# Optimization experiments

Hardware: AMD Instinct MI355X
Metric: run time of the kernel (lower is better)

Reference implementation:

```python
import jax, jax.numpy as jnp
import numpy as np

T, OBS, H, NOBJ = 32768, 256, 512, 4


def _xavier(key, shape):
    fan_in, fan_out = shape[0], shape[1]
    lim = jnp.sqrt(6.0 / (fan_in + fan_out)).astype(jnp.float32)
    return jax.random.uniform(key, shape, jnp.float32, -lim, lim)


def setup_inputs() -> dict:
    key = jax.random.key(0)
    ks = jax.random.split(key, 16)
    # weights stored as [in, out] so y = x @ W (same math as nn.Linear with W.T)
    return {
        "x": jax.random.normal(ks[0], (T, OBS), jnp.float32),
        "W_in0": _xavier(ks[1], (OBS, H)),
        "W_B0": _xavier(ks[2], (OBS, H)),
        "W_C0": _xavier(ks[3], (OBS, H)),
        "W_d0": _xavier(ks[4], (OBS, H)),
        "A_log0": jax.random.normal(ks[5], (H,), jnp.float32),
        "W_in1": _xavier(ks[6], (H, H)),
        "W_B1": _xavier(ks[7], (H, H)),
        "W_C1": _xavier(ks[8], (H, H)),
        "W_d1": _xavier(ks[9], (H, H)),
        "A_log1": jax.random.normal(ks[10], (H,), jnp.float32),
        "W_out": _xavier(ks[11], (H, NOBJ)),
        "b_out": jnp.zeros((NOBJ,), jnp.float32),
        "W_skip": _xavier(ks[12], (OBS, NOBJ)),
    }


def _mamba_layer(x, W_in, W_B, W_C, W_d, A_log):
    # x: [T, D_in] -> [T, H]
    x_state = x @ W_in           # [T, H]
    B = x @ W_B                  # [T, H]
    C = x @ W_C                  # [T, H]
    delta = jax.nn.sigmoid(x @ W_d)  # [T, H]
    A = -jnp.exp(A_log)          # [H]
    A_bar = jnp.exp(delta * A)   # [T, H], in (0, 1)
    Bx = B * x_state             # [T, H]

    def step(h, inp):
        a_t, bx_t = inp
        h = a_t * h + bx_t
        return h, h

    h0 = jnp.zeros((x_state.shape[-1],), x_state.dtype)
    _, h_seq = jax.lax.scan(step, h0, (A_bar, Bx))  # [T, H]
    return C * h_seq


def reference(x, W_in0, W_B0, W_C0, W_d0, A_log0,
              W_in1, W_B1, W_C1, W_d1, A_log1,
              W_out, b_out, W_skip):
    skip = x
    y = _mamba_layer(x, W_in0, W_B0, W_C0, W_d0, A_log0)
    y = _mamba_layer(y, W_in1, W_B1, W_C1, W_d1, A_log1)
    out = y @ W_out + b_out + skip @ W_skip  # [T, NOBJ]
    return out
```

## Files before the change

### kernel.cpp

```cpp
#include <hip/hip_runtime.h>

typedef __attribute__((ext_vector_type(8))) short short8;
typedef __attribute__((ext_vector_type(4))) float floatx4;

#define T_SIZE 32768
#define OBS    256
#define H      512
#define NC     1024
#define CHUNK  32
#define NGRP   64
#define GCH    16

__device__ __forceinline__ unsigned short f2bf(float f){
    union { float f; unsigned u; } v; v.f = f;
    unsigned u = v.u;
    u += 0x7FFFu + ((u >> 16) & 1u);
    return (unsigned short)(u >> 16);
}
__device__ __forceinline__ float bf2f(unsigned short u){
    union { unsigned u; float f; } v; v.u = ((unsigned)u) << 16; return v.f;
}

#define GLOAD_LDS16(g, l) \
    __builtin_amdgcn_global_load_lds((const __attribute__((address_space(1))) unsigned*)(g), \
                                     (__attribute__((address_space(3))) unsigned*)(l), 16, 0, 0)

__global__ void prep_kernel(const float* __restrict__ x, unsigned short* __restrict__ xb,
                            const float* __restrict__ A0W0, const float* __restrict__ A0W1,
                            const float* __restrict__ A0W2, const float* __restrict__ A0W3,
                            unsigned short* __restrict__ Wt0,
                            const float* __restrict__ A1W0, const float* __restrict__ A1W1,
                            const float* __restrict__ A1W2, const float* __restrict__ A1W3,
                            unsigned short* __restrict__ Wt1){
    const int b = blockIdx.x;
    const int tid = threadIdx.x;
    if (b < 8192){
        int i = b * 256 + tid;
        float4 v = ((const float4*)x)[i];
        ushort4 o;
        o.x = f2bf(v.x); o.y = f2bf(v.y); o.z = f2bf(v.z); o.w = f2bf(v.w);
        ((ushort4*)xb)[i] = o;
    } else if (b < 10240){
        const int K = OBS, KH = OBS * H;
        int idx = (b - 8192) * 256 + tid;
        int s   = idx / KH;
        int rem = idx - s * KH;
        int h = rem >> 8;
        int k = rem & 255;
        const float* W = (s == 0) ? A0W0 : (s == 1) ? A0W1 : (s == 2) ? A0W2 : A0W3;
        int bb = h >> 4, hh = h & 15;
        Wt0[(size_t)((bb * 4 + s) * 16 + hh) * K + k] = f2bf(W[(size_t)k * H + h]);
    } else {
        const int K = H, KH = H * H;
        int idx = (b - 10240) * 256 + tid;
        int s   = idx / KH;
        int rem = idx - s * KH;
        int h = rem >> 9;
        int k = rem & 511;
        const float* W = (s == 0) ? A1W0 : (s == 1) ? A1W1 : (s == 2) ? A1W2 : A1W3;
        int bb = h >> 4, hh = h & 15;
        Wt1[(size_t)((bb * 4 + s) * 16 + hh) * K + k] = f2bf(W[(size_t)k * H + h]);
    }
}

template<int K>
__global__ __launch_bounds__(256, 3) void gemm_layer_kernel(
    const unsigned short* __restrict__ xb,
    const unsigned short* __restrict__ wt,
    const float* __restrict__ A_log,
    unsigned short* __restrict__ gT, unsigned short* __restrict__ bxT, unsigned short* __restrict__ CT,
    float* __restrict__ Pbuf, float* __restrict__ Hbuf)
{
    __shared__ unsigned short SM[3][8192];

    const int tid  = threadIdx.x;
    const int wave = tid >> 6;
    const int lane = tid & 63;
    const int ml   = lane & 15;
    const int quad = lane >> 4;
    const int wm   = wave & 1;
    const int wn   = wave >> 1;

    const int flat = blockIdx.y * 16 + blockIdx.x;
    const int xcd  = flat & 7;
    const int j    = flat >> 3;
    const int nb   = j & 15;
    const int mb   = (j >> 4) * 8 + xcd;
    const int m0   = mb * 128;

    const int srow = tid >> 2;
    const int sel  = (((tid & 3) ^ ((tid >> 3) & 3))) * 8;
    const int swz  = (ml >> 1) & 3;

    const unsigned short* pa0 = xb + (size_t)(m0 + srow) * K + sel;
    const unsigned short* pa1 = pa0 + (size_t)64 * K;
    const unsigned short* pb0 = wt + (size_t)(nb * 128 + srow) * K + sel;
    const unsigned short* pb1 = pb0 + (size_t)64 * K;

    const int ldsA0 = (wave * 64 + 0  ) * 8;
    const int ldsA1 = (wave * 64 + 256) * 8;

    const int rbaseA = (wm * 64 + ml) * 32 + (quad ^ swz) * 8;
    const int rbaseB = (wn * 64 + ml) * 32 + (quad ^ swz) * 8;

    floatx4 acc[4][4];
    #pragma unroll
    for (int i = 0; i < 4; i++)
        #pragma unroll
        for (int jj = 0; jj < 4; jj++)
            acc[i][jj] = (floatx4)(0.0f);

    constexpr int NK = K >> 5;

#define STAGE(kt_) { const int b_ = (kt_) % 3; const int ko_ = (kt_) * 32; \
        GLOAD_LDS16(pa0 + ko_, &SM[b_][ldsA0]); \
        GLOAD_LDS16(pa1 + ko_, &SM[b_][ldsA1]); \
        GLOAD_LDS16(pb0 + ko_, &SM[b_][4096 + ldsA0]); \
        GLOAD_LDS16(pb1 + ko_, &SM[b_][4096 + ldsA1]); }

    STAGE(0); STAGE(1);
    asm volatile("s_waitcnt vmcnt(4)" ::: "memory");
    __builtin_amdgcn_s_barrier();
    __builtin_amdgcn_sched_barrier(0);

    #pragma unroll
    for (int kk = 0; kk < NK; ++kk){
        const int cur = kk % 3;

        if (kk + 2 < NK) STAGE(kk + 2);

        short8 av[4], bv[4];
        #pragma unroll
        for (int i = 0; i < 4; i++)
            av[i] = *(const short8*)(&SM[cur][0] + rbaseA + i * 16 * 32);
        #pragma unroll
        for (int jj = 0; jj < 4; jj++)
            bv[jj] = *(const short8*)(&SM[cur][4096] + rbaseB + jj * 16 * 32);

        __builtin_amdgcn_s_setprio(1);
        #pragma unroll
        for (int i = 0; i < 4; i++)
            #pragma unroll
            for (int jj = 0; jj < 4; jj++)
                acc[i][jj] = __builtin_amdgcn_mfma_f32_16x16x32_bf16(av[i], bv[jj], acc[i][jj], 0, 0, 0);
        __builtin_amdgcn_s_setprio(0);

        if (kk + 1 < NK){
            if (kk + 2 < NK) { asm volatile("s_waitcnt vmcnt(4)" ::: "memory"); }
            else             { asm volatile("s_waitcnt vmcnt(0)" ::: "memory"); }
            __builtin_amdgcn_s_barrier();
            __builtin_amdgcn_sched_barrier(0);
        }
    }
    __syncthreads();

#undef STAGE

    unsigned short* SMe = &SM[0][0];
    float2* segbuf = (float2*)(SMe + 12288);
    const int col = wn * 16 + ml;
    const int h   = nb * 32 + col;
    const float Aneg = -expf(A_log[h]);

    #pragma unroll
    for (int i = 0; i < 4; i++){
        float p = 1.0f, hh = 0.0f;
        #pragma unroll
        for (int r = 0; r < 4; r++){
            int trow = wm * 64 + i * 16 + quad * 4 + r;
            float dv = acc[i][3][r];
            float delta = 1.0f / (1.0f + expf(-dv));
            unsigned short gb = f2bf(delta * Aneg);
            float a = __expf(bf2f(gb));
            unsigned short bb = f2bf(acc[i][1][r] * acc[i][0][r]);
            SMe[        trow * 32 + col] = gb;
            SMe[4096 +  trow * 32 + col] = bb;
            SMe[8192 +  trow * 32 + col] = f2bf(acc[i][2][r]);
            hh = fmaf(a, hh, bf2f(bb));
            p *= a;
        }
        const int ch = wm * 2 + (i >> 1);
        const int s  = (i & 1) * 4 + quad;
        segbuf[(ch * 8 + s) * 32 + col] = make_float2(p, hh);
    }
    __syncthreads();
    {
        const short8* s8 = (const short8*)SMe;
        #pragma unroll
        for (int arr = 0; arr < 3; arr++){
            unsigned short* bp = (arr == 0) ? gT : (arr == 1) ? bxT : CT;
            #pragma unroll
            for (int half = 0; half < 2; half++){
                int u = half * 256 + tid;
                int row = u >> 2, part = u & 3;
                *(short8*)(bp + (size_t)(m0 + row) * H + nb * 32 + part * 8) = s8[arr * 512 + u];
            }
        }
    }
    if (tid < 128){
        const int ccol = tid & 31, ch = tid >> 5;
        float P = 1.0f, Hc = 0.0f;
        #pragma unroll
        for (int s = 0; s < 8; s++){
            float2 ph = segbuf[(ch * 8 + s) * 32 + ccol];
            Hc = fmaf(ph.x, Hc, ph.y);
            P *= ph.x;
        }
        const int c = mb * 4 + ch;
        Pbuf[(size_t)c * H + nb * 32 + ccol] = P;
        Hbuf[(size_t)c * H + nb * 32 + ccol] = Hc;
    }
}

__global__ void scan2a_kernel(const float* __restrict__ P, const float* __restrict__ Hc,
                              float* __restrict__ Pg, float* __restrict__ Hg){
    const int g  = blockIdx.x;
    const int j4 = threadIdx.x * 4;
    float4 pc = {1.f,1.f,1.f,1.f}, hc = {0.f,0.f,0.f,0.f};
    #pragma unroll
    for (int i = 0; i < GCH; i++){
        size_t o = (size_t)(g * GCH + i) * H + j4;
        float4 P4 = *(const float4*)(P + o);
        float4 H4 = *(const float4*)(Hc + o);
        hc.x = fmaf(P4.x, hc.x, H4.x); pc.x *= P4.x;
        hc.y = fmaf(P4.y, hc.y, H4.y); pc.y *= P4.y;
        hc.z = fmaf(P4.z, hc.z, H4.z); pc.z *= P4.z;
        hc.w = fmaf(P4.w, hc.w, H4.w); pc.w *= P4.w;
    }
    *(float4*)(Pg + (size_t)g * H + j4) = pc;
    *(float4*)(Hg + (size_t)g * H + j4) = hc;
}

__global__ __launch_bounds__(256) void scan3_kernel(
    const unsigned short* __restrict__ gT, const unsigned short* __restrict__ bxT,
    const unsigned short* __restrict__ CT,
    const float* __restrict__ P, const float* __restrict__ Hc,
    const float* __restrict__ Pg, const float* __restrict__ Hg,
    unsigned short* __restrict__ yb){
    const int c  = blockIdx.x;
    const int j2 = threadIdx.x * 2;
    const int grp = c >> 4;
    float2 h = {0.f, 0.f};
    for (int g = 0; g < grp; ++g){
        float2 P2 = *(const float2*)(Pg + (size_t)g * H + j2);
        float2 H2 = *(const float2*)(Hg + (size_t)g * H + j2);
        h.x = fmaf(P2.x, h.x, H2.x);
        h.y = fmaf(P2.y, h.y, H2.y);
    }
    for (int cc = grp << 4; cc < c; ++cc){
        float2 P2 = *(const float2*)(P + (size_t)cc * H + j2);
        float2 H2 = *(const float2*)(Hc + (size_t)cc * H + j2);
        h.x = fmaf(P2.x, h.x, H2.x);
        h.y = fmaf(P2.y, h.y, H2.y);
    }
    size_t off = (size_t)c * CHUNK * H + j2;
    #pragma unroll 8
    for (int i = 0; i < CHUNK; i++){
        ushort2 gv = *(const ushort2*)(gT + off);
        ushort2 bv = *(const ushort2*)(bxT + off);
        ushort2 cv = *(const ushort2*)(CT + off);
        h.x = fmaf(__expf(bf2f(gv.x)), h.x, bf2f(bv.x));
        h.y = fmaf(__expf(bf2f(gv.y)), h.y, bf2f(bv.y));
        ushort2 o;
        o.x = f2bf(bf2f(cv.x) * h.x);
        o.y = f2bf(bf2f(cv.y) * h.y);
        *(ushort2*)(yb + off) = o;
        off += H;
    }
}

__global__ __launch_bounds__(256) void scan3f_kernel(
    const unsigned short* __restrict__ gT, const unsigned short* __restrict__ bxT,
    const unsigned short* __restrict__ CT,
    const float* __restrict__ P, const float* __restrict__ Hc,
    const float* __restrict__ Pg, const float* __restrict__ Hg,
    const unsigned short* __restrict__ xb,
    const float* __restrict__ Wout, const float* __restrict__ bout,
    const float* __restrict__ Wskip,
    float* __restrict__ out){
    __shared__ unsigned short ystage[32 * 512];
    const int tid = threadIdx.x;
    const int c   = blockIdx.x;
    const int j2  = tid * 2;
    const int grp = c >> 4;
    float2 h = {0.f, 0.f};
    for (int g = 0; g < grp; ++g){
        float2 P2 = *(const float2*)(Pg + (size_t)g * H + j2);
        float2 H2 = *(const float2*)(Hg + (size_t)g * H + j2);
        h.x = fmaf(P2.x, h.x, H2.x);
        h.y = fmaf(P2.y, h.y, H2.y);
    }
    for (int cc = grp << 4; cc < c; ++cc){
        float2 P2 = *(const float2*)(P + (size_t)cc * H + j2);
        float2 H2 = *(const float2*)(Hc + (size_t)cc * H + j2);
        h.x = fmaf(P2.x, h.x, H2.x);
        h.y = fmaf(P2.y, h.y, H2.y);
    }
    size_t off = (size_t)c * CHUNK * H + j2;
    #pragma unroll 8
    for (int i = 0; i < CHUNK; i++){
        ushort2 gv = *(const ushort2*)(gT + off);
        ushort2 bv = *(const ushort2*)(bxT + off);
        ushort2 cv = *(const ushort2*)(CT + off);
        h.x = fmaf(__expf(bf2f(gv.x)), h.x, bf2f(bv.x));
        h.y = fmaf(__expf(bf2f(gv.y)), h.y, bf2f(bv.y));
        ushort2 o;
        o.x = f2bf(bf2f(cv.x) * h.x);
        o.y = f2bf(bf2f(cv.y) * h.y);
        *(ushort2*)(&ystage[i * 512 + j2]) = o;
        off += H;
    }
    __syncthreads();

    const int wave = tid >> 6;
    const int lane = tid & 63;
    const float4* W4 = (const float4*)Wout;
    const float4* S4 = (const float4*)Wskip;
    const float b0 = bout[0], b1 = bout[1], b2 = bout[2], b3 = bout[3];
    for (int rr = 0; rr < 8; ++rr){
        const int r = wave * 8 + rr;
        const int t = c * 32 + r;
        float s0 = 0.f, s1 = 0.f, s2 = 0.f, s3 = 0.f;
        #pragma unroll
        for (int k = lane; k < H; k += 64){
            float yv = bf2f(ystage[r * 512 + k]);
            float4 w = W4[k];
            s0 = fmaf(yv, w.x, s0); s1 = fmaf(yv, w.y, s1);
            s2 = fmaf(yv, w.z, s2); s3 = fmaf(yv, w.w, s3);
        }
        #pragma unroll
        for (int k = lane; k < OBS; k += 64){
            float xv = bf2f(xb[(size_t)t * OBS + k]);
            float4 w = S4[k];
            s0 = fmaf(xv, w.x, s0); s1 = fmaf(xv, w.y, s1);
            s2 = fmaf(xv, w.z, s2); s3 = fmaf(xv, w.w, s3);
        }
        #pragma unroll
        for (int o = 32; o > 0; o >>= 1){
            s0 += __shfl_down(s0, o);
            s1 += __shfl_down(s1, o);
            s2 += __shfl_down(s2, o);
            s3 += __shfl_down(s3, o);
        }
        if (lane == 0){
            out[(size_t)t * 4 + 0] = s0 + b0;
            out[(size_t)t * 4 + 1] = s1 + b1;
            out[(size_t)t * 4 + 2] = s2 + b2;
            out[(size_t)t * 4 + 3] = s3 + b3;
        }
    }
}

extern "C" void kernel_launch(void* const* d_in, const int* in_sizes, int n_in,
                              void* d_out, int out_size, void* d_ws, size_t ws_size,
                              hipStream_t stream)
{
    const float* x     = (const float*)d_in[0];
    const float* W_in0 = (const float*)d_in[1];
    const float* W_B0  = (const float*)d_in[2];
    const float* W_C0  = (const float*)d_in[3];
    const float* W_d0  = (const float*)d_in[4];
    const float* A0    = (const float*)d_in[5];
    const float* W_in1 = (const float*)d_in[6];
    const float* W_B1  = (const float*)d_in[7];
    const float* W_C1  = (const float*)d_in[8];
    const float* W_d1  = (const float*)d_in[9];
    const float* A1    = (const float*)d_in[10];
    const float* Wout  = (const float*)d_in[11];
    const float* bout  = (const float*)d_in[12];
    const float* Wskip = (const float*)d_in[13];
    float* out = (float*)d_out;

    char* ws = (char*)d_ws;
    size_t off = 0;
    auto alloc = [&](size_t bytes) -> void* {
        void* p = ws + off;
        off += (bytes + 255) & ~(size_t)255;
        return p;
    };
    unsigned short* xb  = (unsigned short*)alloc((size_t)T_SIZE * OBS * 2);
    unsigned short* yb  = (unsigned short*)alloc((size_t)T_SIZE * H * 2);
    unsigned short* Wt0 = (unsigned short*)alloc((size_t)4 * H * OBS * 2);
    unsigned short* Wt1 = (unsigned short*)alloc((size_t)4 * H * H * 2);
    unsigned short* gT  = (unsigned short*)alloc((size_t)T_SIZE * H * 2);
    unsigned short* bxT = (unsigned short*)alloc((size_t)T_SIZE * H * 2);
    unsigned short* CT  = (unsigned short*)alloc((size_t)T_SIZE * H * 2);
    float* Pbuf = (float*)alloc((size_t)NC * H * 4);
    float* Hbuf = (float*)alloc((size_t)NC * H * 4);
    float* Pg   = (float*)alloc((size_t)NGRP * H * 4);
    float* Hg   = (float*)alloc((size_t)NGRP * H * 4);
    (void)ws_size; (void)in_sizes; (void)n_in; (void)out_size;

    prep_kernel<<<14336, 256, 0, stream>>>(x, xb,
                                           W_in0, W_B0, W_C0, W_d0, Wt0,
                                           W_in1, W_B1, W_C1, W_d1, Wt1);

    dim3 ggrid(16, 256);

    gemm_layer_kernel<OBS><<<ggrid, 256, 0, stream>>>(xb, Wt0, A0, gT, bxT, CT, Pbuf, Hbuf);
    scan2a_kernel<<<NGRP, 128, 0, stream>>>(Pbuf, Hbuf, Pg, Hg);
    scan3_kernel<<<NC, 256, 0, stream>>>(gT, bxT, CT, Pbuf, Hbuf, Pg, Hg, yb);

    gemm_layer_kernel<H><<<ggrid, 256, 0, stream>>>(yb, Wt1, A1, gT, bxT, CT, Pbuf, Hbuf);
    scan2a_kernel<<<NGRP, 128, 0, stream>>>(Pbuf, Hbuf, Pg, Hg);
    scan3f_kernel<<<NC, 256, 0, stream>>>(gT, bxT, CT, Pbuf, Hbuf, Pg, Hg,
                                          xb, Wout, bout, Wskip, out);
}
```

Before: 308.2 us.

## Split each scan chunk into two half-chunks with mid-chunk carry states

The GEMM epilogue now also writes the partial prefix state for the first half of each 32-step chunk (Pm/Hm). The scan kernels then have each block's threads cover 4 columns by 16 timesteps instead of 2 columns by 32 timesteps, with the second half seeded from the mid-chunk state. This halves the serial dependency length per thread and widens loads to 8-byte vectors. The cost is extra global writes and reads for the mid-chunk buffers, plus duplicated prefix-combine work across both halves.

```diff
diff --git a/kernel.cpp b/kernel.cpp
--- a/kernel.cpp
+++ b/kernel.cpp
@@ -69,7 +69,8 @@
     const unsigned short* __restrict__ wt,
     const float* __restrict__ A_log,
     unsigned short* __restrict__ gT, unsigned short* __restrict__ bxT, unsigned short* __restrict__ CT,
-    float* __restrict__ Pbuf, float* __restrict__ Hbuf)
+    float* __restrict__ Pbuf, float* __restrict__ Hbuf,
+    float* __restrict__ Pm, float* __restrict__ Hm)
 {
     __shared__ unsigned short SM[3][8192];
 
@@ -199,14 +200,22 @@
     }
     if (tid < 128){
         const int ccol = tid & 31, ch = tid >> 5;
+        const int c = mb * 4 + ch;
         float P = 1.0f, Hc = 0.0f;
         #pragma unroll
-        for (int s = 0; s < 8; s++){
+        for (int s = 0; s < 4; s++){
             float2 ph = segbuf[(ch * 8 + s) * 32 + ccol];
             Hc = fmaf(ph.x, Hc, ph.y);
             P *= ph.x;
         }
-        const int c = mb * 4 + ch;
+        Pm[(size_t)c * H + nb * 32 + ccol] = P;
+        Hm[(size_t)c * H + nb * 32 + ccol] = Hc;
+        #pragma unroll
+        for (int s = 4; s < 8; s++){
+            float2 ph = segbuf[(ch * 8 + s) * 32 + ccol];
+            Hc = fmaf(ph.x, Hc, ph.y);
+            P *= ph.x;
+        }
         Pbuf[(size_t)c * H + nb * 32 + ccol] = P;
         Hbuf[(size_t)c * H + nb * 32 + ccol] = Hc;
     }
@@ -235,36 +244,54 @@
     const unsigned short* __restrict__ gT, const unsigned short* __restrict__ bxT,
     const unsigned short* __restrict__ CT,
     const float* __restrict__ P, const float* __restrict__ Hc,
+    const float* __restrict__ Pm, const float* __restrict__ Hm,
     const float* __restrict__ Pg, const float* __restrict__ Hg,
     unsigned short* __restrict__ yb){
-    const int c  = blockIdx.x;
-    const int j2 = threadIdx.x * 2;
-    const int grp = c >> 4;
-    float2 h = {0.f, 0.f};
+    const int c    = blockIdx.x;
+    const int half = threadIdx.x >> 7;
+    const int j4   = (threadIdx.x & 127) * 4;
+    const int grp  = c >> 4;
+    float4 h = {0.f, 0.f, 0.f, 0.f};
     for (int g = 0; g < grp; ++g){
-        float2 P2 = *(const float2*)(Pg + (size_t)g * H + j2);
-        float2 H2 = *(const float2*)(Hg + (size_t)g * H + j2);
-        h.x = fmaf(P2.x, h.x, H2.x);
-        h.y = fmaf(P2.y, h.y, H2.y);
+        float4 P4 = *(const float4*)(Pg + (size_t)g * H + j4);
+        float4 H4 = *(const float4*)(Hg + (size_t)g * H + j4);
+        h.x = fmaf(P4.x, h.x, H4.x);
+        h.y = fmaf(P4.y, h.y, H4.y);
+        h.z = fmaf(P4.z, h.z, H4.z);
+        h.w = fmaf(P4.w, h.w, H4.w);
     }
     for (int cc = grp << 4; cc < c; ++cc){
-        float2 P2 = *(const float2*)(P + (size_t)cc * H + j2);
-        float2 H2 = *(const float2*)(Hc + (size_t)cc * H + j2);
-        h.x = fmaf(P2.x, h.x, H2.x);
-        h.y = fmaf(P2.y, h.y, H2.y);
-    }
-    size_t off = (size_t)c * CHUNK * H + j2;
+        float4 P4 = *(const float4*)(P + (size_t)cc * H + j4);
+        float4 H4 = *(const float4*)(Hc + (size_t)cc * H + j4);
+        h.x = fmaf(P4.x, h.x, H4.x);
+        h.y = fmaf(P4.y, h.y, H4.y);
+        h.z = fmaf(P4.z, h.z, H4.z);
+        h.w = fmaf(P4.w, h.w, H4.w);
+    }
+    if (half){
+        float4 P4 = *(const float4*)(Pm + (size_t)c * H + j4);
+        float4 H4 = *(const float4*)(Hm + (size_t)c * H + j4);
+        h.x = fmaf(P4.x, h.x, H4.x);
+        h.y = fmaf(P4.y, h.y, H4.y);
+        h.z = fmaf(P4.z, h.z, H4.z);
+        h.w = fmaf(P4.w, h.w, H4.w);
+    }
+    size_t off = (size_t)(c * CHUNK + half * 16) * H + j4;
     #pragma unroll 8
-    for (int i = 0; i < CHUNK; i++){
-        ushort2 gv = *(const ushort2*)(gT + off);
-        ushort2 bv = *(const ushort2*)(bxT + off);
-        ushort2 cv = *(const ushort2*)(CT + off);
+    for (int i = 0; i < 16; i++){
+        ushort4 gv = *(const ushort4*)(gT + off);
+        ushort4 bv = *(const ushort4*)(bxT + off);
+        ushort4 cv = *(const ushort4*)(CT + off);
         h.x = fmaf(__expf(bf2f(gv.x)), h.x, bf2f(bv.x));
         h.y = fmaf(__expf(bf2f(gv.y)), h.y, bf2f(bv.y));
-        ushort2 o;
+        h.z = fmaf(__expf(bf2f(gv.z)), h.z, bf2f(bv.z));
+        h.w = fmaf(__expf(bf2f(gv.w)), h.w, bf2f(bv.w));
+        ushort4 o;
         o.x = f2bf(bf2f(cv.x) * h.x);
         o.y = f2bf(bf2f(cv.y) * h.y);
-        *(ushort2*)(yb + off) = o;
+        o.z = f2bf(bf2f(cv.z) * h.z);
+        o.w = f2bf(bf2f(cv.w) * h.w);
+        *(ushort4*)(yb + off) = o;
         off += H;
     }
 }
@@ -273,41 +300,59 @@
     const unsigned short* __restrict__ gT, const unsigned short* __restrict__ bxT,
     const unsigned short* __restrict__ CT,
     const float* __restrict__ P, const float* __restrict__ Hc,
+    const float* __restrict__ Pm, const float* __restrict__ Hm,
     const float* __restrict__ Pg, const float* __restrict__ Hg,
     const unsigned short* __restrict__ xb,
     const float* __restrict__ Wout, const float* __restrict__ bout,
     const float* __restrict__ Wskip,
     float* __restrict__ out){
     __shared__ unsigned short ystage[32 * 512];
-    const int tid = threadIdx.x;
-    const int c   = blockIdx.x;
-    const int j2  = tid * 2;
-    const int grp = c >> 4;
-    float2 h = {0.f, 0.f};
+    const int tid  = threadIdx.x;
+    const int c    = blockIdx.x;
+    const int half = tid >> 7;
+    const int j4   = (tid & 127) * 4;
+    const int grp  = c >> 4;
+    float4 h = {0.f, 0.f, 0.f, 0.f};
     for (int g = 0; g < grp; ++g){
-        float2 P2 = *(const float2*)(Pg + (size_t)g * H + j2);
-        float2 H2 = *(const float2*)(Hg + (size_t)g * H + j2);
-        h.x = fmaf(P2.x, h.x, H2.x);
-        h.y = fmaf(P2.y, h.y, H2.y);
+        float4 P4 = *(const float4*)(Pg + (size_t)g * H + j4);
+        float4 H4 = *(const float4*)(Hg + (size_t)g * H + j4);
+        h.x = fmaf(P4.x, h.x, H4.x);
+        h.y = fmaf(P4.y, h.y, H4.y);
+        h.z = fmaf(P4.z, h.z, H4.z);
+        h.w = fmaf(P4.w, h.w, H4.w);
     }
     for (int cc = grp << 4; cc < c; ++cc){
-        float2 P2 = *(const float2*)(P + (size_t)cc * H + j2);
-        float2 H2 = *(const float2*)(Hc + (size_t)cc * H + j2);
-        h.x = fmaf(P2.x, h.x, H2.x);
-        h.y = fmaf(P2.y, h.y, H2.y);
-    }
-    size_t off = (size_t)c * CHUNK * H + j2;
+        float4 P4 = *(const float4*)(P + (size_t)cc * H + j4);
+        float4 H4 = *(const float4*)(Hc + (size_t)cc * H + j4);
+        h.x = fmaf(P4.x, h.x, H4.x);
+        h.y = fmaf(P4.y, h.y, H4.y);
+        h.z = fmaf(P4.z, h.z, H4.z);
+        h.w = fmaf(P4.w, h.w, H4.w);
+    }
+    if (half){
+        float4 P4 = *(const float4*)(Pm + (size_t)c * H + j4);
+        float4 H4 = *(const float4*)(Hm + (size_t)c * H + j4);
+        h.x = fmaf(P4.x, h.x, H4.x);
+        h.y = fmaf(P4.y, h.y, H4.y);
+        h.z = fmaf(P4.z, h.z, H4.z);
+        h.w = fmaf(P4.w, h.w, H4.w);
+    }
+    size_t off = (size_t)(c * CHUNK + half * 16) * H + j4;
     #pragma unroll 8
-    for (int i = 0; i < CHUNK; i++){
-        ushort2 gv = *(const ushort2*)(gT + off);
-        ushort2 bv = *(const ushort2*)(bxT + off);
-        ushort2 cv = *(const ushort2*)(CT + off);
+    for (int i = 0; i < 16; i++){
+        ushort4 gv = *(const ushort4*)(gT + off);
+        ushort4 bv = *(const ushort4*)(bxT + off);
+        ushort4 cv = *(const ushort4*)(CT + off);
         h.x = fmaf(__expf(bf2f(gv.x)), h.x, bf2f(bv.x));
         h.y = fmaf(__expf(bf2f(gv.y)), h.y, bf2f(bv.y));
-        ushort2 o;
+        h.z = fmaf(__expf(bf2f(gv.z)), h.z, bf2f(bv.z));
+        h.w = fmaf(__expf(bf2f(gv.w)), h.w, bf2f(bv.w));
+        ushort4 o;
         o.x = f2bf(bf2f(cv.x) * h.x);
         o.y = f2bf(bf2f(cv.y) * h.y);
-        *(ushort2*)(&ystage[i * 512 + j2]) = o;
+        o.z = f2bf(bf2f(cv.z) * h.z);
+        o.w = f2bf(bf2f(cv.w) * h.w);
+        *(ushort4*)(&ystage[(half * 16 + i) * 512 + j4]) = o;
         off += H;
     }
     __syncthreads();
@@ -387,6 +432,8 @@
     unsigned short* CT  = (unsigned short*)alloc((size_t)T_SIZE * H * 2);
     float* Pbuf = (float*)alloc((size_t)NC * H * 4);
     float* Hbuf = (float*)alloc((size_t)NC * H * 4);
+    float* Pm   = (float*)alloc((size_t)NC * H * 4);
+    float* Hm   = (float*)alloc((size_t)NC * H * 4);
     float* Pg   = (float*)alloc((size_t)NGRP * H * 4);
     float* Hg   = (float*)alloc((size_t)NGRP * H * 4);
     (void)ws_size; (void)in_sizes; (void)n_in; (void)out_size;
@@ -397,12 +444,12 @@
 
     dim3 ggrid(16, 256);
 
-    gemm_layer_kernel<OBS><<<ggrid, 256, 0, stream>>>(xb, Wt0, A0, gT, bxT, CT, Pbuf, Hbuf);
+    gemm_layer_kernel<OBS><<<ggrid, 256, 0, stream>>>(xb, Wt0, A0, gT, bxT, CT, Pbuf, Hbuf, Pm, Hm);
     scan2a_kernel<<<NGRP, 128, 0, stream>>>(Pbuf, Hbuf, Pg, Hg);
-    scan3_kernel<<<NC, 256, 0, stream>>>(gT, bxT, CT, Pbuf, Hbuf, Pg, Hg, yb);
-
-    gemm_layer_kernel<H><<<ggrid, 256, 0, stream>>>(yb, Wt1, A1, gT, bxT, CT, Pbuf, Hbuf);
+    scan3_kernel<<<NC, 256, 0, stream>>>(gT, bxT, CT, Pbuf, Hbuf, Pm, Hm, Pg, Hg, yb);
+
+    gemm_layer_kernel<H><<<ggrid, 256, 0, stream>>>(yb, Wt1, A1, gT, bxT, CT, Pbuf, Hbuf, Pm, Hm);
     scan2a_kernel<<<NGRP, 128, 0, stream>>>(Pbuf, Hbuf, Pg, Hg);
-    scan3f_kernel<<<NC, 256, 0, stream>>>(gT, bxT, CT, Pbuf, Hbuf, Pg, Hg,
+    scan3f_kernel<<<NC, 256, 0, stream>>>(gT, bxT, CT, Pbuf, Hbuf, Pm, Hm, Pg, Hg,
                                           xb, Wout, bout, Wskip, out);
 }
```

Measured after the change: 313.3 us. No clear change (+1.6%).
